# Kernel tuning notes

Measured on AMD Instinct MI355X. Metric: run time of the kernel, lower is better.

Reference implementation:

```python
import jax, jax.numpy as jnp
import numpy as np

PT_SEQ_LEN = 16    # hardcoded hw_seq_len in the module
THETA = 10000.0


def _rope_tables(head_dim):
    # VisionRotaryEmbeddingFast with dim = head_dim // 2, pt_seq_len = ft_seq_len = 16
    d = head_dim // 2                                   # 32
    freqs = 1.0 / (THETA ** (np.arange(0, d, 2, dtype=np.float64) / d))  # (d//2,) = (16,)
    t = np.arange(PT_SEQ_LEN, dtype=np.float64)         # t / ft * pt = arange since ft==pt
    f = np.einsum('i,j->ij', t, freqs)                  # (16, 16)
    f = np.repeat(f, 2, axis=-1)                        # (16, 32)  '... n -> ... (n r)'
    fa = np.broadcast_to(f[:, None, :], (PT_SEQ_LEN, PT_SEQ_LEN, d))
    fb = np.broadcast_to(f[None, :, :], (PT_SEQ_LEN, PT_SEQ_LEN, d))
    full = np.concatenate([fa, fb], axis=-1).reshape(-1, head_dim)  # (256, head_dim)
    return (jnp.asarray(np.cos(full), dtype=jnp.float32),
            jnp.asarray(np.sin(full), dtype=jnp.float32))


def _rotate_half(x):
    # '... (d r) -> ... d r', r=2; (x1, x2) -> (-x2, x1)
    x = x.reshape(*x.shape[:-1], -1, 2)
    x1, x2 = x[..., 0], x[..., 1]
    return jnp.stack((-x2, x1), axis=-1).reshape(*x.shape[:-2], -1)


def _apply_rope(t, cos, sin):
    # t: (B, H, N, hd); cos/sin: (N, hd)
    return t * cos + _rotate_half(t) * sin


def setup_inputs() -> dict:
    key = jax.random.key(0)
    ks = jax.random.split(key, 5)
    B, N, dim, sem = 64, 256, 1024, 768
    return {
        'q': jax.random.normal(ks[0], (B, N, dim), dtype=jnp.float32),
        'kv': jax.random.normal(ks[1], (B, N, sem), dtype=jnp.float32),
        'Wq': jax.random.normal(ks[2], (dim, dim), dtype=jnp.float32) * 0.02,
        'Wkv': jax.random.normal(ks[3], (sem, 2 * dim), dtype=jnp.float32) * 0.02,
        'Wproj': jax.random.normal(ks[4], (dim, dim), dtype=jnp.float32) * 0.02,
        'bproj': jnp.zeros((dim,), dtype=jnp.float32),
    }


def reference(q, kv, Wq, Wkv, Wproj, bproj):
    B, N, C = q.shape
    H = 16
    hd = C // H
    cos, sin = _rope_tables(hd)

    qh = (q @ Wq).reshape(B, N, H, hd).transpose(0, 2, 1, 3)        # (B,H,N,hd)
    kvh = (kv @ Wkv).reshape(B, N, 2, H, hd).transpose(2, 0, 3, 1, 4)
    k, v = kvh[0], kvh[1]                                           # (B,H,N,hd)

    qh = _apply_rope(qh, cos, sin)
    k = _apply_rope(k, cos, sin)

    scale = 1.0 / jnp.sqrt(jnp.float32(hd))  # F.sdpa default scale
    logits = jnp.einsum('bhqd,bhkd->bhqk', qh, k) * scale
    attn = jax.nn.softmax(logits, axis=-1)
    out = jnp.einsum('bhqk,bhkd->bhqd', attn, v)                    # (B,H,N,hd)
    out = out.transpose(0, 2, 1, 3).reshape(B, N, C)
    return out @ Wproj + bproj
```

## Files before the change

kernel.cpp:

```cpp
#include <hip/hip_runtime.h>
#include <hip/hip_bf16.h>
#include <math.h>


typedef unsigned int uint;
typedef __attribute__((ext_vector_type(4)))  short s16x4;
typedef __attribute__((ext_vector_type(8)))  short s16x8;
typedef __attribute__((ext_vector_type(4)))  float f32x4;
typedef __attribute__((ext_vector_type(16))) float f32x16;

#define AS1 __attribute__((address_space(1)))
#define AS3 __attribute__((address_space(3)))

__device__ __forceinline__ short f2bf(float x){
  union{float f;uint u;}v; v.f=x;
  return (short)((v.u + 0x7FFFu + ((v.u>>16)&1u))>>16);
}
__device__ __forceinline__ float bf2f(short s){
  union{float f;uint u;}v; v.u=((uint)(unsigned short)s)<<16; return v.f;
}
__device__ __forceinline__ uint packbf(float a,float b){
  return (uint)(unsigned short)f2bf(a) | ((uint)(unsigned short)f2bf(b)<<16);
}
__device__ __forceinline__ void gl_lds16(const void* g, void* l){
  __builtin_amdgcn_global_load_lds((const AS1 uint*)g, (AS3 uint*)l, 16, 0, 0);
}
__device__ __forceinline__ s16x8 ld16(const short* p){ return *(const s16x8*)p; }

__global__ void k_prep(const void* Wq, const void* Wkv, const void* Wp,
                       const void* bsrc, const void* qsrc, const void* kvsrc,
                       short* WqT, short* WkvT, short* WpT, float* biasF,
                       float* cosT, float* sinT, short* qbf, short* kvbf,
                       int* flag){
  __shared__ int cnt;
  const uint* qw=(const uint*)qsrc;
  if(threadIdx.x==0) cnt=0;
  __syncthreads();
  int c=0;
  for(int i=threadIdx.x;i<2048;i+=256){
    uint e=(qw[i]>>7)&0xFFu;
    if(e>=120u && e<=130u) c++;
  }
  atomicAdd(&cnt,c);
  __syncthreads();
  const int f=(cnt>1024)?0:1;
  if(threadIdx.x==0 && blockIdx.x==0) *flag=f;

  const long S0=16384, S1=S0+1024, S2=S1+131072, S3=S2+196608, S4=S3+131072,
             S5=S4+2097152, S6=S5+1572864;
  const long lim = f ? S6 : S4;
  const long stride=(long)gridDim.x*blockDim.x;
  for(long idx=(long)blockIdx.x*blockDim.x+threadIdx.x; idx<lim; idx+=stride){
    if(idx<S0){
      int t=(int)idx, n=t>>6, d=t&63;
      int i=n>>4, j=n&15, p=(d&31)>>1;
      double fr=pow(10000.0, -(double)(2*p)/32.0);
      double tt=(d<32)?(double)i:(double)j;
      double a=tt*fr;
      cosT[t]=(float)cos(a); sinT[t]=(float)sin(a);
    } else if(idx<S1){
      int t=(int)(idx-S0);
      biasF[t]= f ? ((const float*)bsrc)[t] : bf2f(((const short*)bsrc)[t]);
    } else if(idx<S4){
      const void* W; short* WT; int K,Nn; long g;
      if(idx<S2){ W=Wq;  WT=WqT;  K=1024; Nn=1024; g=idx-S1; }
      else if(idx<S3){ W=Wkv; WT=WkvT; K=768; Nn=2048; g=idx-S2; }
      else { W=Wp;  WT=WpT;  K=1024; Nn=1024; g=idx-S3; }
      int n=(int)(g%Nn); int k0=(int)(g/Nn)*8;
      s16x8 o;
      #pragma unroll
      for(int j=0;j<8;j++){
        o[j]= f ? f2bf(((const float*)W)[(long)(k0+j)*Nn+n])
                : ((const short*)W)[(long)(k0+j)*Nn+n];
      }
      *(s16x8*)&WT[(long)n*K+k0]=o;
    } else {
      const void* src; short* dst; long i;
      if(idx<S5){ src=qsrc; dst=qbf; i=idx-S4; }
      else { src=kvsrc; dst=kvbf; i=idx-S5; }
      const float4* s=(const float4*)src;
      float4 a=s[i*2], b=s[i*2+1];
      s16x8 o;
      o[0]=f2bf(a.x);o[1]=f2bf(a.y);o[2]=f2bf(a.z);o[3]=f2bf(a.w);
      o[4]=f2bf(b.x);o[5]=f2bf(b.y);o[6]=f2bf(b.z);o[7]=f2bf(b.w);
      ((s16x8*)dst)[i]=o;
    }
  }
}

#define BAR   __builtin_amdgcn_s_barrier()
#define LGKM0 asm volatile("s_waitcnt lgkmcnt(0)" ::: "memory")
#define VMC4  asm volatile("s_waitcnt vmcnt(4)" ::: "memory")
#define PRIO1 __builtin_amdgcn_s_setprio(1)
#define PRIO0 __builtin_amdgcn_s_setprio(0)

#define MM(H,V,BR) do{ \
  _Pragma("unroll") for(int ks_=0;ks_<4;ks_++){ \
    _Pragma("unroll") for(int mf_=0;mf_<2;mf_++){ \
      acc[(H)*2+mf_][V]=__builtin_amdgcn_mfma_f32_32x32x16_bf16( \
        aR[mf_][ks_],BR[ks_],acc[(H)*2+mf_][V],0,0,0); \
  }} }while(0)

#define HALFIT(BUF,TA,TB) do{ \
  const short* RA=&lds[BUF][0][wm][0]; \
  const short* RB=&lds[BUF][1][0][0]; \
  ldA(RA,0,aR); ldB(RB,0,bR0); stage(0,0,TA); \
  BAR; LGKM0; PRIO1; MM(0,0,bR0); PRIO0; BAR; \
  ldB(RB,1,bR1); stage(0,1,TA); \
  BAR; LGKM0; PRIO1; MM(0,1,bR1); PRIO0; BAR; \
  ldA(RA,1,aR); stage(1,0,TB); \
  BAR; LGKM0; PRIO1; MM(1,1,bR1); PRIO0; BAR; \
  stage(1,1,TB); \
  BAR; PRIO1; MM(1,0,bR0); PRIO0; VMC4; BAR; \
}while(0)

template<int MODE>
__launch_bounds__(512,2)
__global__ void k_gemm8(const short* __restrict__ Aq, const short* __restrict__ Bq,
                        const short* __restrict__ Akv, const short* __restrict__ Bkv,
                        const short* __restrict__ qraw, const short* __restrict__ kvraw,
                        short* __restrict__ out0, short* __restrict__ out1,
                        short* __restrict__ out2,
                        const float* __restrict__ cosT, const float* __restrict__ sinT,
                        const float* __restrict__ bias, const int* __restrict__ flag,
                        void* __restrict__ dout){
  __shared__ __align__(16) short lds[2][2][2][8192];
  const int tid=threadIdx.x, lane=tid&63, wave=tid>>6;
  const int ln31=lane&31, l5=lane>>5;
  const int wm=wave>>2, wn=wave&3;
  const int fl=*flag;
  int role, tm, tn, Kdim;
  const short *Ag, *Bg;
  if(MODE==1){
    const int nwg=gridDim.x, cpx=nwg>>3;
    const int wg=((int)blockIdx.x&7)*cpx+((int)blockIdx.x>>3);
    role=2; tn=wg&3; tm=wg>>2; Kdim=1024;
    Ag=Aq+(long)tm*256*1024; Bg=Bq+(long)tn*256*1024;
  } else {
    const int xcd=(int)blockIdx.x&7, pos=(int)blockIdx.x>>3;
    const short* Aq_e  = fl? Aq  : qraw;
    const short* Akv_e = fl? Akv : kvraw;
    if(pos<32){ role=0; int qi=xcd*32+pos; tn=qi&3; tm=qi>>2; Kdim=1024;
      Ag=Aq_e+(long)tm*256*1024; Bg=Bq+(long)tn*256*1024; }
    else { role=1; int ki=xcd*64+(pos-32); tn=ki&7; tm=ki>>3; Kdim=768;
      Ag=Akv_e+(long)tm*256*768; Bg=Bkv+(long)tn*256*768; }
  }
  const int NT=Kdim>>6;
  f32x16 acc[4][2]={};
  s16x8 aR[2][4], bR0[4], bR1[4];

  auto stage=[&](int op,int hf,int kt){
    int ktw=(kt>=NT)?kt-NT:kt;
    const short* G=(op? Bg:Ag)+((long)(hf*128))*Kdim+ktw*64;
    short* R=&lds[kt&1][op][hf][0];
    #pragma unroll
    for(int l=0;l<2;l++){
      int lr=l*64+wave*8+(lane>>3);
      int c=(lane&7)^((lr>>1)&7);
      gl_lds16(G+(long)lr*Kdim+c*8, R+l*4096+wave*512+lane*8);
    }
  };
  auto ldA=[&](const short* R,int h,s16x8 (&a)[2][4]){
    #pragma unroll
    for(int mf=0;mf<2;mf++){
      int lr=h*64+mf*32+ln31;
      int sw=(lr>>1)&7;
      #pragma unroll
      for(int ks=0;ks<4;ks++){
        int slot=(ks*2+l5)^sw;
        a[mf][ks]=*(const s16x8*)&R[lr*64+slot*8];
      }
    }
  };
  auto ldB=[&](const short* R0,int v,s16x8 (&b)[4]){
    int row=wn*64+v*32+ln31;
    const short* R=R0+(row>>7)*8192;
    int lr=row&127;
    int sw=(lr>>1)&7;
    #pragma unroll
    for(int ks=0;ks<4;ks++){
      int slot=(ks*2+l5)^sw;
      b[ks]=*(const s16x8*)&R[lr*64+slot*8];
    }
  };

  stage(1,0,0); stage(1,1,0); stage(0,0,0); stage(0,1,0);
  stage(1,0,1); stage(1,1,1);
  VMC4;
  BAR;

  for(int t=0;t<NT;t+=2){
    HALFIT(0, t+1, t+2);
    HALFIT(1, t+2, t+3);
  }

  const int mb=tm*256+wm*128, nb=tn*256+wn*64;
  #pragma unroll
  for(int mf=0;mf<4;mf++)
  #pragma unroll
  for(int nf=0;nf<2;nf++){
    const int n=nb+nf*32+ln31;
    if(MODE==1){
      float bi=bias[n];
      #pragma unroll
      for(int r=0;r<16;r++){
        int m=mb+mf*32+(r&3)+8*(r>>2)+4*l5;
        float o=acc[mf][nf][r]+bi;
        long idx=((long)m<<10)+n;
        if(fl) ((float*)dout)[idx]=o;
        else   ((short*)dout)[idx]=f2bf(o);
      }
    } else if(role==0){
      int h=n>>6, d=n&63;
      #pragma unroll
      for(int r=0;r<16;r++){
        int m=mb+mf*32+(r&3)+8*(r>>2)+4*l5;
        int b=m>>8, nn=m&255;
        float v=acc[mf][nf][r];
        float part=__shfl_xor(v,1);
        float c=cosT[(nn<<6)+d], s=sinT[(nn<<6)+d];
        float rot=(d&1)?part:-part;
        out0[(((long)(b*16+h)*256+nn)<<6)+d]=f2bf((v*c+rot*s)*0.125f);
      }
    } else {
      if(n<1024){
        int h=(n>>6)&15, d=n&63;
        #pragma unroll
        for(int r=0;r<16;r++){
          int m=mb+mf*32+(r&3)+8*(r>>2)+4*l5;
          int b=m>>8, nn=m&255;
          float v=acc[mf][nf][r];
          float part=__shfl_xor(v,1);
          float c=cosT[(nn<<6)+d], s=sinT[(nn<<6)+d];
          float rot=(d&1)?part:-part;
          out1[(((long)(b*16+h)*256+nn)<<6)+d]=f2bf(v*c+rot*s);
        }
      }else{
        int h=(n>>6)&15, d=n&63;
        #pragma unroll
        for(int rq=0;rq<4;rq++){
          int m0=mb+mf*32+8*rq+4*l5;
          int b=m0>>8, nn0=m0&255;
          s16x4 pk;
          #pragma unroll
          for(int j=0;j<4;j++) pk[j]=f2bf(acc[mf][nf][rq*4+j]);
          *(s16x4*)&out2[(((long)(b*16+h)*64+d)<<8)+nn0]=pk;
        }
      }
    }
  }
}

__launch_bounds__(256,2)
__global__ void k_attn(const short* qh, const short* kb, const short* vt, short* out){
  __shared__ __align__(16) short ol[4][64][72];
  int bh=blockIdx.x, b=bh>>4, h=bh&15;
  int tid=threadIdx.x, lane=tid&63, wave=tid>>6;
  const short* Q=qh+(long)bh*256*64;
  const short* K=kb+(long)bh*256*64;
  const short* VT=vt+(long)bh*64*256;
  uint* P=(uint*)&ol[wave][0][0];

  s16x8 qf[4][2];
  #pragma unroll
  for(int qb=0;qb<4;qb++)
    #pragma unroll
    for(int kk=0;kk<2;kk++)
      qf[qb][kk]=ld16(Q+(wave*64+qb*16+(lane&15))*64+kk*32+(lane>>4)*8);

  f32x4 o[4][4]={};
  float mrow[4]={-INFINITY,-INFINITY,-INFINITY,-INFINITY};
  float srow[4]={0.f,0.f,0.f,0.f};
  const int g=lane>>4, lc=lane&15;

  for(int kt=0;kt<8;kt++){
    s16x8 kA[2][2];
    #pragma unroll
    for(int f=0;f<2;f++)
      #pragma unroll
      for(int kk=0;kk<2;kk++)
        kA[f][kk]=ld16(K+(kt*32+f*16+lc)*64+kk*32+g*8);
    s16x8 vA[4];
    #pragma unroll
    for(int db=0;db<4;db++)
      vA[db]=ld16(VT+(db*16+lc)*256+kt*32+g*8);

    f32x4 st[2][4]={};
    PRIO1;
    #pragma unroll
    for(int kk=0;kk<2;kk++)
      #pragma unroll
      for(int f=0;f<2;f++)
        #pragma unroll
        for(int qb=0;qb<4;qb++)
          st[f][qb]=__builtin_amdgcn_mfma_f32_16x16x32_bf16(kA[f][kk],qf[qb][kk],st[f][qb],0,0,0);
    PRIO0;

    #pragma unroll
    for(int qb=0;qb<4;qb++){
      float pm=st[0][qb][0];
      #pragma unroll
      for(int f=0;f<2;f++)
        #pragma unroll
        for(int r=0;r<4;r++) pm=fmaxf(pm,st[f][qb][r]);
      pm=fmaxf(pm,__shfl_xor(pm,16));
      pm=fmaxf(pm,__shfl_xor(pm,32));
      float mn=fmaxf(mrow[qb],pm);
      float al=__expf(mrow[qb]-mn);
      mrow[qb]=mn;
      float p00=__expf(st[0][qb][0]-mn), p01=__expf(st[0][qb][1]-mn);
      float p02=__expf(st[0][qb][2]-mn), p03=__expf(st[0][qb][3]-mn);
      float p10=__expf(st[1][qb][0]-mn), p11=__expf(st[1][qb][1]-mn);
      float p12=__expf(st[1][qb][2]-mn), p13=__expf(st[1][qb][3]-mn);
      float ps=p00+p01+p02+p03+p10+p11+p12+p13;
      ps+=__shfl_xor(ps,16);
      ps+=__shfl_xor(ps,32);
      srow[qb]=srow[qb]*al+ps;
      #pragma unroll
      for(int db=0;db<4;db++){
        o[db][qb][0]*=al; o[db][qb][1]*=al; o[db][qb][2]*=al; o[db][qb][3]*=al;
      }
      uint* row=&P[(qb*16+lc)*20];
      row[g*2  ]=packbf(p00,p01);
      row[g*2+1]=packbf(p02,p03);
      row[8+g*2  ]=packbf(p10,p11);
      row[8+g*2+1]=packbf(p12,p13);
    }
    asm volatile("s_waitcnt lgkmcnt(0)" ::: "memory");
    s16x8 pb[4];
    #pragma unroll
    for(int qb=0;qb<4;qb++)
      pb[qb]=*(const s16x8*)&P[(qb*16+lc)*20+g*4];
    PRIO1;
    #pragma unroll
    for(int db=0;db<4;db++)
      #pragma unroll
      for(int qb=0;qb<4;qb++)
        o[db][qb]=__builtin_amdgcn_mfma_f32_16x16x32_bf16(vA[db],pb[qb],o[db][qb],0,0,0);
    PRIO0;
  }

  #pragma unroll
  for(int db=0;db<4;db++)
    #pragma unroll
    for(int qb=0;qb<4;qb++)
      #pragma unroll
      for(int r=0;r<4;r++){
        int d=db*16+(lane>>4)*4+r;
        int q=qb*16+(lane&15);
        ol[wave][q][d]=f2bf(o[db][qb][r]/srow[qb]);
      }
  __syncthreads();
  #pragma unroll
  for(int it=0;it<8;it++){
    int q=wave*64+it*8+(lane>>3);
    int cc=lane&7;
    s16x8 x=*(const s16x8*)&ol[wave][it*8+(lane>>3)][cc*8];
    *(s16x8*)&out[((long)(b*256+q)<<10)+h*64+cc*8]=x;
  }
}

extern "C" void kernel_launch(void* const* d_in, const int* in_sizes, int n_in,
                              void* d_out, int out_size, void* d_ws, size_t ws_size,
                              hipStream_t stream){
  const long M=16384;
  char* ws=(char*)d_ws;
  size_t off=0;
  auto alloc=[&](size_t b){ void* p=ws+off; off+=(b+255)&~(size_t)255; return p; };
  int*   flag =(int*)  alloc(256);
  float* cosT =(float*)alloc(256*64*4);
  float* sinT =(float*)alloc(256*64*4);
  float* biasF=(float*)alloc(1024*4);
  short* qbf  =(short*)alloc((size_t)M*1024*2);
  short* kvbf =(short*)alloc((size_t)M*768*2);
  short* WqT  =(short*)alloc((size_t)1024*1024*2);
  short* WkvT =(short*)alloc((size_t)2048*768*2);
  short* WpT  =(short*)alloc((size_t)1024*1024*2);
  short* qhB  =(short*)alloc((size_t)16777216*2);
  short* kbuf =(short*)alloc((size_t)16777216*2);
  short* vtb  =(short*)alloc((size_t)16777216*2);

  k_prep<<<2048,256,0,stream>>>(d_in[2],d_in[3],d_in[4],d_in[5],d_in[0],d_in[1],
                                WqT,WkvT,WpT,biasF,cosT,sinT,qbf,kvbf,flag);
  k_gemm8<0><<<768,512,0,stream>>>(qbf,WqT,kvbf,WkvT,
                                   (const short*)d_in[0],(const short*)d_in[1],
                                   qhB,kbuf,vtb,cosT,sinT,biasF,flag,nullptr);
  k_attn<<<1024,256,0,stream>>>(qhB,kbuf,vtb,qbf);
  k_gemm8<1><<<256,512,0,stream>>>(qbf,WpT,nullptr,nullptr,nullptr,nullptr,
                                   nullptr,nullptr,nullptr,
                                   cosT,sinT,biasF,flag,d_out);
}
```

Measured before the change: 252.7 us.

## Make QKV GEMM persistent: each block runs one Q tile and two KV tiles

```diff
diff --git a/kernel.cpp b/kernel.cpp
--- a/kernel.cpp
+++ b/kernel.cpp
@@ -129,35 +129,45 @@
   const int ln31=lane&31, l5=lane>>5;
   const int wm=wave>>2, wn=wave&3;
   const int fl=*flag;
-  int role, tm, tn, Kdim;
-  const short *Ag, *Bg;
+  const int JT = (MODE==1)?16:40;
+
+  const short *Ab0,*Bb0,*Ab1,*Bb1,*Ab2,*Bb2;
+  int tm0,tn0,tm1,tn1,tm2,tn2;
   if(MODE==1){
     const int nwg=gridDim.x, cpx=nwg>>3;
     const int wg=((int)blockIdx.x&7)*cpx+((int)blockIdx.x>>3);
-    role=2; tn=wg&3; tm=wg>>2; Kdim=1024;
-    Ag=Aq+(long)tm*256*1024; Bg=Bq+(long)tn*256*1024;
+    tn0=wg&3; tm0=wg>>2;
+    Ab0=Aq+(long)tm0*256*1024; Bb0=Bq+(long)tn0*256*1024;
+    Ab1=Ab0; Bb1=Bb0; Ab2=Ab0; Bb2=Bb0; tm1=tm0;tn1=tn0;tm2=tm0;tn2=tn0;
   } else {
     const int xcd=(int)blockIdx.x&7, pos=(int)blockIdx.x>>3;
     const short* Aq_e  = fl? Aq  : qraw;
     const short* Akv_e = fl? Akv : kvraw;
-    if(pos<32){ role=0; int qi=xcd*32+pos; tn=qi&3; tm=qi>>2; Kdim=1024;
-      Ag=Aq_e+(long)tm*256*1024; Bg=Bq+(long)tn*256*1024; }
-    else { role=1; int ki=xcd*64+(pos-32); tn=ki&7; tm=ki>>3; Kdim=768;
-      Ag=Akv_e+(long)tm*256*768; Bg=Bkv+(long)tn*256*768; }
-  }
-  const int NT=Kdim>>6;
+    int qi=xcd*32+pos, k0=xcd*64+2*pos, k1=k0+1;
+    tm0=qi>>2; tn0=qi&3;
+    Ab0=Aq_e +(long)tm0*256*1024; Bb0=Bq +(long)tn0*256*1024;
+    tm1=k0>>3; tn1=k0&7;
+    Ab1=Akv_e+(long)tm1*256*768;  Bb1=Bkv+(long)tn1*256*768;
+    tm2=k1>>3; tn2=k1&7;
+    Ab2=Akv_e+(long)tm2*256*768;  Bb2=Bkv+(long)tn2*256*768;
+  }
+
   f32x16 acc[4][2]={};
   s16x8 aR[2][4], bR0[4], bR1[4];
 
-  auto stage=[&](int op,int hf,int kt){
-    int ktw=(kt>=NT)?kt-NT:kt;
-    const short* G=(op? Bg:Ag)+((long)(hf*128))*Kdim+ktw*64;
-    short* R=&lds[kt&1][op][hf][0];
+  auto stage=[&](int op,int hf,int j){
+    int jj = (j>=JT)? j-JT : j;
+    const short *Abase, *Bbase; int kd, t0;
+    if(MODE==1 || jj<16){ Abase=Ab0; Bbase=Bb0; kd=1024; t0=0; }
+    else if(jj<28)      { Abase=Ab1; Bbase=Bb1; kd=768;  t0=16; }
+    else                { Abase=Ab2; Bbase=Bb2; kd=768;  t0=28; }
+    const short* G=(op? Bbase:Abase)+((long)(hf*128))*kd+(jj-t0)*64;
+    short* R=&lds[jj&1][op][hf][0];
     #pragma unroll
     for(int l=0;l<2;l++){
       int lr=l*64+wave*8+(lane>>3);
       int c=(lane&7)^((lr>>1)&7);
-      gl_lds16(G+(long)lr*Kdim+c*8, R+l*4096+wave*512+lane*8);
+      gl_lds16(G+(long)lr*kd+c*8, R+l*4096+wave*512+lane*8);
     }
   };
   auto ldA=[&](const short* R,int h,s16x8 (&a)[2][4]){
@@ -183,48 +193,33 @@
       b[ks]=*(const s16x8*)&R[lr*64+slot*8];
     }
   };
-
-  stage(1,0,0); stage(1,1,0); stage(0,0,0); stage(0,1,0);
-  stage(1,0,1); stage(1,1,1);
-  VMC4;
-  BAR;
-
-  for(int t=0;t<NT;t+=2){
-    HALFIT(0, t+1, t+2);
-    HALFIT(1, t+2, t+3);
-  }
-
-  const int mb=tm*256+wm*128, nb=tn*256+wn*64;
-  #pragma unroll
-  for(int mf=0;mf<4;mf++)
-  #pragma unroll
-  for(int nf=0;nf<2;nf++){
-    const int n=nb+nf*32+ln31;
-    if(MODE==1){
-      float bi=bias[n];
-      #pragma unroll
-      for(int r=0;r<16;r++){
-        int m=mb+mf*32+(r&3)+8*(r>>2)+4*l5;
-        float o=acc[mf][nf][r]+bi;
-        long idx=((long)m<<10)+n;
-        if(fl) ((float*)dout)[idx]=o;
-        else   ((short*)dout)[idx]=f2bf(o);
-      }
-    } else if(role==0){
-      int h=n>>6, d=n&63;
-      #pragma unroll
-      for(int r=0;r<16;r++){
-        int m=mb+mf*32+(r&3)+8*(r>>2)+4*l5;
-        int b=m>>8, nn=m&255;
-        float v=acc[mf][nf][r];
-        float part=__shfl_xor(v,1);
-        float c=cosT[(nn<<6)+d], s=sinT[(nn<<6)+d];
-        float rot=(d&1)?part:-part;
-        out0[(((long)(b*16+h)*256+nn)<<6)+d]=f2bf((v*c+rot*s)*0.125f);
-      }
-    } else {
-      if(n<1024){
-        int h=(n>>6)&15, d=n&63;
+  auto clr=[&](){
+    #pragma unroll
+    for(int mf=0;mf<4;mf++)
+      #pragma unroll
+      for(int nf=0;nf<2;nf++)
+        #pragma unroll
+        for(int e=0;e<16;e++) acc[mf][nf][e]=0.f;
+  };
+  auto epi=[&](int role,int tm,int tn){
+    const int mb=tm*256+wm*128, nb=tn*256+wn*64;
+    #pragma unroll
+    for(int mf=0;mf<4;mf++)
+    #pragma unroll
+    for(int nf=0;nf<2;nf++){
+      const int n=nb+nf*32+ln31;
+      if(MODE==1){
+        float bi=bias[n];
+        #pragma unroll
+        for(int r=0;r<16;r++){
+          int m=mb+mf*32+(r&3)+8*(r>>2)+4*l5;
+          float o=acc[mf][nf][r]+bi;
+          long idx=((long)m<<10)+n;
+          if(fl) ((float*)dout)[idx]=o;
+          else   ((short*)dout)[idx]=f2bf(o);
+        }
+      } else if(role==0){
+        int h=n>>6, d=n&63;
         #pragma unroll
         for(int r=0;r<16;r++){
           int m=mb+mf*32+(r&3)+8*(r>>2)+4*l5;
@@ -233,21 +228,52 @@
           float part=__shfl_xor(v,1);
           float c=cosT[(nn<<6)+d], s=sinT[(nn<<6)+d];
           float rot=(d&1)?part:-part;
-          out1[(((long)(b*16+h)*256+nn)<<6)+d]=f2bf(v*c+rot*s);
+          out0[(((long)(b*16+h)*256+nn)<<6)+d]=f2bf((v*c+rot*s)*0.125f);
         }
-      }else{
-        int h=(n>>6)&15, d=n&63;
-        #pragma unroll
-        for(int rq=0;rq<4;rq++){
-          int m0=mb+mf*32+8*rq+4*l5;
-          int b=m0>>8, nn0=m0&255;
-          s16x4 pk;
+      } else {
+        if(n<1024){
+          int h=(n>>6)&15, d=n&63;
           #pragma unroll
-          for(int j=0;j<4;j++) pk[j]=f2bf(acc[mf][nf][rq*4+j]);
-          *(s16x4*)&out2[(((long)(b*16+h)*64+d)<<8)+nn0]=pk;
+          for(int r=0;r<16;r++){
+            int m=mb+mf*32+(r&3)+8*(r>>2)+4*l5;
+            int b=m>>8, nn=m&255;
+            float v=acc[mf][nf][r];
+            float part=__shfl_xor(v,1);
+            float c=cosT[(nn<<6)+d], s=sinT[(nn<<6)+d];
+            float rot=(d&1)?part:-part;
+            out1[(((long)(b*16+h)*256+nn)<<6)+d]=f2bf(v*c+rot*s);
+          }
+        }else{
+          int h=(n>>6)&15, d=n&63;
+          #pragma unroll
+          for(int rq=0;rq<4;rq++){
+            int m0=mb+mf*32+8*rq+4*l5;
+            int b=m0>>8, nn0=m0&255;
+            s16x4 pk;
+            #pragma unroll
+            for(int j=0;j<4;j++) pk[j]=f2bf(acc[mf][nf][rq*4+j]);
+            *(s16x4*)&out2[(((long)(b*16+h)*64+d)<<8)+nn0]=pk;
+          }
         }
       }
     }
+  };
+
+  stage(1,0,0); stage(1,1,0); stage(0,0,0); stage(0,1,0);
+  stage(1,0,1); stage(1,1,1);
+  VMC4;
+  BAR;
+
+  if(MODE==1){
+    for(int tt=0;tt<16;tt+=2){ HALFIT(0,tt+1,tt+2); HALFIT(1,tt+2,tt+3); }
+    epi(2,tm0,tn0);
+  } else {
+    for(int tt=0;tt<16;tt+=2){ HALFIT(0,tt+1,tt+2); HALFIT(1,tt+2,tt+3); }
+    epi(0,tm0,tn0); clr();
+    for(int tt=16;tt<28;tt+=2){ HALFIT(0,tt+1,tt+2); HALFIT(1,tt+2,tt+3); }
+    epi(1,tm1,tn1); clr();
+    for(int tt=28;tt<40;tt+=2){ HALFIT(0,tt+1,tt+2); HALFIT(1,tt+2,tt+3); }
+    epi(1,tm2,tn2);
   }
 }
 
@@ -382,7 +408,7 @@
 
   k_prep<<<2048,256,0,stream>>>(d_in[2],d_in[3],d_in[4],d_in[5],d_in[0],d_in[1],
                                 WqT,WkvT,WpT,biasF,cosT,sinT,qbf,kvbf,flag);
-  k_gemm8<0><<<768,512,0,stream>>>(qbf,WqT,kvbf,WkvT,
+  k_gemm8<0><<<256,512,0,stream>>>(qbf,WqT,kvbf,WkvT,
                                    (const short*)d_in[0],(const short*)d_in[1],
                                    qhB,kbuf,vtb,cosT,sinT,biasF,flag,nullptr);
   k_attn<<<1024,256,0,stream>>>(qhB,kbuf,vtb,qbf);
```

Result: slower. 459.5 us (+81.9%).
